# Optimization experiments

Hardware: AMD Instinct MI355X
Metric: run time of the kernel (lower is better)

The kernel has to match this reference:

```python
import jax, jax.numpy as jnp
import numpy as np

LOG2 = float(np.log(2.0))
CUTOFF = 10.0
NUM_G = 50
NUM_MOLS = 512


def ssp(x):
    # ShiftedSoftplus: softplus(x) - log(2)
    return jax.nn.softplus(x) - LOG2


def setup_inputs() -> dict:
    key = jax.random.key(0)
    ks = jax.random.split(key, 12)
    MOLS, ATOMS, K, H, F, G, L = NUM_MOLS, 64, 32, 128, 128, NUM_G, 6
    N = MOLS * ATOMS
    # structured radius graph: node i connects to (local+1..K) mod ATOMS in its molecule
    node = np.arange(N)
    mol = node // ATOMS
    loc = node % ATOMS
    dlt = np.arange(1, K + 1)
    src = ((loc[:, None] + dlt[None, :]) % ATOMS + mol[:, None] * ATOMS).reshape(-1)
    dst = np.repeat(node, K)
    edge_index = jnp.asarray(np.stack([src, dst]), dtype=jnp.int32)  # [2, E]
    z = jax.random.randint(ks[0], (N,), 0, 100, dtype=jnp.int32)
    # positions in a 5A cube -> all intra-molecule dists < cutoff=10
    pos = jax.random.uniform(ks[1], (N, 3), dtype=jnp.float32) * 5.0
    batch = jnp.asarray(mol, dtype=jnp.int32)

    def nrm(k, shape, scale):
        return jax.random.normal(k, shape, dtype=jnp.float32) * scale

    return dict(
        z=z, pos=pos, batch=batch, edge_index=edge_index,
        emb=nrm(ks[2], (100, H), 1.0),
        mlp_w1=nrm(ks[3], (L, G, F), 0.14),
        mlp_b1=jnp.zeros((L, F), jnp.float32),
        mlp_w2=nrm(ks[4], (L, F, F), 0.09),
        mlp_b2=jnp.zeros((L, F), jnp.float32),
        conv_w1=nrm(ks[5], (L, H, F), 0.09),
        conv_w2=nrm(ks[6], (L, F, H), 0.09),
        conv_b2=jnp.zeros((L, H), jnp.float32),
        lin_w=nrm(ks[7], (L, H, H), 0.09),
        lin_b=jnp.zeros((L, H), jnp.float32),
        out_w1=nrm(ks[8], (H, H // 2), 0.1),
        out_b1=jnp.zeros((H // 2,), jnp.float32),
        out_w2=nrm(ks[9], (H // 2, 1), 0.15),
        out_b2=jnp.zeros((1,), jnp.float32),
    )


def reference(z, pos, batch, edge_index, emb, mlp_w1, mlp_b1, mlp_w2, mlp_b2,
              conv_w1, conv_w2, conv_b2, lin_w, lin_b,
              out_w1, out_b1, out_w2, out_b2):
    N = pos.shape[0]
    src, dst = edge_index[0], edge_index[1]  # source j -> target i
    h = emb[z]                                                 # [N,H]
    d = jnp.linalg.norm(pos[dst] - pos[src], axis=-1)          # [E]
    # GaussianSmearing(start=0, stop=cutoff, num_gaussians)
    offset = jnp.linspace(0.0, CUTOFF, NUM_G)
    coeff = -0.5 / (offset[1] - offset[0]) ** 2
    edge_attr = jnp.exp(coeff * (d[:, None] - offset[None, :]) ** 2)  # [E,G]
    # cosine cutoff
    C = 0.5 * (jnp.cos(d * jnp.pi / CUTOFF) + 1.0)             # [E]
    L = mlp_w1.shape[0]
    for l in range(L):  # fixed small layer count
        # filter MLP on edge features, modulated by cutoff
        W = (ssp(edge_attr @ mlp_w1[l] + mlp_b1[l]) @ mlp_w2[l] + mlp_b2[l]) * C[:, None]  # [E,F]
        hx = h @ conv_w1[l]                                    # lin1 (no bias) [N,F]
        msg = hx[src] * W                                      # gather + modulate [E,F]
        agg = jax.ops.segment_sum(msg, dst, num_segments=N)    # scatter-add [N,F]
        v = agg @ conv_w2[l] + conv_b2[l]                      # lin2
        v = ssp(v) @ lin_w[l] + lin_b[l]                       # act + lin
        h = h + v                                              # residual
    h = ssp(h @ out_w1 + out_b1)
    h = h @ out_w2 + out_b2                                    # [N,1]
    out = jax.ops.segment_sum(h, batch, num_segments=NUM_MOLS) # per-molecule 'add' readout
    return out
```

## Files before the change

kernel.cpp:

```cpp
#include <hip/hip_runtime.h>
#include <math.h>

#define NN 32768
#define HH 128
#define GG 50
#define KK 32
#define LL 6
#define MM 512
#define TT 2048
#define TROWS 2049
#define ROWB 256

typedef _Float16 f16x8 __attribute__((ext_vector_type(8)));
typedef float    f32x4 __attribute__((ext_vector_type(4)));

__device__ __forceinline__ float ssp(float x) {
  return fmaxf(x, 0.f) + __logf(1.f + __expf(-fabsf(x))) - 0.69314718055994530942f;
}

__global__ __launch_bounds__(256)
void setup_all(const float* __restrict__ cw1, const float* __restrict__ cw2,
               const float* __restrict__ lw, _Float16* __restrict__ cwT,
               const float* __restrict__ mw1, const float* __restrict__ mw2,
               const float* __restrict__ mb1, const float* __restrict__ mb2,
               const float* __restrict__ ow1,
               _Float16* __restrict__ o1hT, _Float16* __restrict__ o1lT,
               char* __restrict__ Vtb) {
  int b = blockIdx.x;
  int tid = threadIdx.x;

  if (b < 72) {
    __shared__ float t[32][33];
    int wid = b >> 2, tj = b & 3;
    int l = wid / 3, m = wid % 3;
    const float* w = ((m == 0) ? cw1 : (m == 1) ? cw2 : lw) + (size_t)l * 16384;
    _Float16* o = cwT + (size_t)wid * 16384;
    int tx = tid & 31, ty = tid >> 5;
    for (int tf = 0; tf < 4; ++tf) {
      __syncthreads();
      for (int r = ty; r < 32; r += 8) t[r][tx] = w[(size_t)(tj*32 + r)*128 + tf*32 + tx];
      __syncthreads();
      for (int r = ty; r < 32; r += 8)
        o[(size_t)(tf*32 + r)*128 + tj*32 + tx] = (_Float16)t[tx][r];
    }
    return;
  }
  if (b < 76) {
    __shared__ float t[32][33];
    int tj = b - 72;
    int tx = tid & 31, ty = tid >> 5;
    for (int tf = 0; tf < 2; ++tf) {
      __syncthreads();
      for (int r = ty; r < 32; r += 8) t[r][tx] = ow1[(size_t)(tj*32 + r)*64 + tf*32 + tx];
      __syncthreads();
      for (int r = ty; r < 32; r += 8) {
        float v = t[tx][r];
        _Float16 h = (_Float16)v;
        size_t oi = (size_t)(tf*32 + r)*128 + tj*32 + tx;
        o1hT[oi] = h;
        o1lT[oi] = (_Float16)(v - (float)h);
      }
    }
    return;
  }

  __shared__ _Float16 eah[16][72], eal[16][72];
  __shared__ _Float16 t1h[16][136], t1l[16][136];

  int bb = b - 76;
  int l  = bb / 129;
  int rb = (bb % 129) * 16;
  int wave = tid >> 6, lane = tid & 63;
  int q = lane >> 4, c = lane & 15;

  const float DSTEP = 10.f / (float)TT;
  const float GSTEP = 10.f / 49.f;
  const float COEFF = -0.5f * 4.9f * 4.9f;

  for (int o = tid; o < 16*64; o += 256) {
    int r = o >> 6, g = o & 63;
    float d = (float)(rb + r) * DSTEP;
    float tt = d - (float)g * GSTEP;
    float v = (g < GG) ? __expf(COEFF * tt * tt) : 0.f;
    _Float16 h = (_Float16)v;
    eah[r][g] = h;
    eal[r][g] = (_Float16)(v - (float)h);
  }
  __syncthreads();

  #pragma unroll
  for (int tI = 0; tI < 2; ++tI) {
    int col = (wave*2 + tI)*16 + c;
    f32x4 a = {0.f, 0.f, 0.f, 0.f};
    #pragma unroll
    for (int kk = 0; kk < 2; ++kk) {
      f16x8 bh, bl;
      #pragma unroll
      for (int i = 0; i < 8; ++i) {
        int k = kk*32 + q*8 + i;
        float v = (k < GG) ? mw1[((size_t)l*GG + k)*128 + col] : 0.f;
        _Float16 h = (_Float16)v;
        bh[i] = h;
        bl[i] = (_Float16)(v - (float)h);
      }
      f16x8 ah = *(const f16x8*)&eah[c][kk*32 + q*8];
      f16x8 al = *(const f16x8*)&eal[c][kk*32 + q*8];
      a = __builtin_amdgcn_mfma_f32_16x16x32_f16(ah, bh, a, 0, 0, 0);
      a = __builtin_amdgcn_mfma_f32_16x16x32_f16(ah, bl, a, 0, 0, 0);
      a = __builtin_amdgcn_mfma_f32_16x16x32_f16(al, bh, a, 0, 0, 0);
    }
    float bv = mb1[l*128 + col];
    #pragma unroll
    for (int r = 0; r < 4; ++r) {
      float v = ssp(a[r] + bv);
      _Float16 h = (_Float16)v;
      t1h[q*4 + r][col] = h;
      t1l[q*4 + r][col] = (_Float16)(v - (float)h);
    }
  }
  __syncthreads();

  #pragma unroll
  for (int tI = 0; tI < 2; ++tI) {
    int col = (wave*2 + tI)*16 + c;
    f32x4 a = {0.f, 0.f, 0.f, 0.f};
    #pragma unroll
    for (int kk = 0; kk < 4; ++kk) {
      f16x8 bh, bl;
      #pragma unroll
      for (int i = 0; i < 8; ++i) {
        int k = kk*32 + q*8 + i;
        float v = mw2[((size_t)l*128 + k)*128 + col];
        _Float16 h = (_Float16)v;
        bh[i] = h;
        bl[i] = (_Float16)(v - (float)h);
      }
      f16x8 ah = *(const f16x8*)&t1h[c][kk*32 + q*8];
      f16x8 al = *(const f16x8*)&t1l[c][kk*32 + q*8];
      a = __builtin_amdgcn_mfma_f32_16x16x32_f16(ah, bh, a, 0, 0, 0);
      a = __builtin_amdgcn_mfma_f32_16x16x32_f16(ah, bl, a, 0, 0, 0);
      a = __builtin_amdgcn_mfma_f32_16x16x32_f16(al, bh, a, 0, 0, 0);
    }
    float bv = mb2[l*128 + col];
    #pragma unroll
    for (int r = 0; r < 4; ++r) {
      int rr = rb + q*4 + r;
      if (rr <= TT) {
        float d = (float)rr * DSTEP;
        float Cc = 0.5f * (__cosf(d * 0.31415926535897931f) + 1.f);
        ((_Float16*)(Vtb + ((size_t)l*TROWS + rr) * ROWB))[col] = (_Float16)((a[r] + bv) * Cc);
      }
    }
  }
}

__device__ __forceinline__ void wave_gemm(const _Float16 (*__restrict__ A)[136],
                                          const _Float16* __restrict__ B,
                                          int c, int q, int n0, f32x4* res) {
  f16x8 bf[4];
  #pragma unroll
  for (int kk = 0; kk < 4; ++kk)
    bf[kk] = *(const f16x8*)&B[(size_t)(n0 + c)*128 + kk*32 + q*8];
  #pragma unroll
  for (int m = 0; m < 4; ++m) {
    f32x4 a = {0.f, 0.f, 0.f, 0.f};
    #pragma unroll
    for (int kk = 0; kk < 4; ++kk) {
      f16x8 av = *(const f16x8*)&A[m*16 + c][kk*32 + q*8];
      a = __builtin_amdgcn_mfma_f32_16x16x32_f16(av, bf[kk], a, 0, 0, 0);
    }
    res[m] = a;
  }
}

__global__ __launch_bounds__(512, 4)
void mega_kernel(const int* __restrict__ z, const float* __restrict__ pos,
                 const float* __restrict__ emb,
                 const _Float16* __restrict__ cwT,
                 const float* __restrict__ cb2, const float* __restrict__ lb,
                 const char* __restrict__ Vtb,
                 const _Float16* __restrict__ o1hT, const _Float16* __restrict__ o1lT,
                 const float* __restrict__ ob1,
                 const float* __restrict__ ow2, const float* __restrict__ ob2,
                 float* __restrict__ out) {
  __shared__ _Float16     hcur[64][136];
  __shared__ _Float16     sb[64][136];
  __shared__ _Float16     hxs[64][136];
  __shared__ float        posL[64][4];
  __shared__ unsigned int edata[64*33];
  __shared__ float        red2[2][64];

  int tid = threadIdx.x;
  int wave = tid >> 6, lane = tid & 63;
  int q = lane >> 4, c = lane & 15;
  int n0 = wave * 16;
  int mol = blockIdx.x, gbase = mol * 64;

  if (tid < 192) posL[tid / 3][tid % 3] = pos[(size_t)gbase*3 + tid];
  for (int o = tid; o < 64*64; o += 512) {
    int n = o >> 6, p2 = (o & 63) * 2;
    float2 ev = *(const float2*)&emb[(size_t)z[gbase + n]*128 + p2];
    hcur[n][p2]     = (_Float16)ev.x;
    hcur[n][p2 + 1] = (_Float16)ev.y;
  }
  __syncthreads();

  for (int e = tid; e < 2048; e += 512) {
    int n = e >> 5, k = e & 31;
    int s = (n + k + 1) & 63;
    float dx = posL[n][0] - posL[s][0];
    float dy = posL[n][1] - posL[s][1];
    float dz = posL[n][2] - posL[s][2];
    float d = sqrtf(dx*dx + dy*dy + dz*dz);
    int idx = (int)(d * ((float)TT / 10.f) + 0.5f);
    edata[n*33 + k] = (unsigned int)idx << 8;
  }
  __syncthreads();

  int en = tid >> 3, ej = tid & 7;
  int f0 = ej * 8;

  for (int l = 0; l < LL; ++l) {
    {
      f32x4 res[4];
      wave_gemm(hcur, cwT + (size_t)(l*3 + 0)*16384, c, q, n0, res);
      #pragma unroll
      for (int m = 0; m < 4; ++m)
        #pragma unroll
        for (int r = 0; r < 4; ++r)
          hxs[m*16 + q*4 + r][n0 + c] = (_Float16)res[m][r];
    }
    __syncthreads();

    f16x8 accA0 = {0,0,0,0,0,0,0,0}, accA1 = accA0;
    f16x8 accB0 = accA0, accB1 = accA0;
    const char* Vl = Vtb + (size_t)l * TROWS * ROWB + f0*2;
    #pragma unroll 4
    for (int k = 0; k < KK; ++k) {
      unsigned int off = edata[en*33 + k];
      int s = (en + k + 1) & 63;
      const char* p = Vl + off;
      f16x8 va = *(const f16x8*)p;
      f16x8 vb = *(const f16x8*)(p + 128);
      f16x8 ha = *(const f16x8*)&hxs[s][f0];
      f16x8 hb = *(const f16x8*)&hxs[s][f0 + 64];
      if (k & 1) { accA1 = ha * va + accA1; accB1 = hb * vb + accB1; }
      else       { accA0 = ha * va + accA0; accB0 = hb * vb + accB0; }
    }
    *(f16x8*)&sb[en][f0]      = accA0 + accA1;
    *(f16x8*)&sb[en][f0 + 64] = accB0 + accB1;
    __syncthreads();

    {
      f32x4 vres[4];
      wave_gemm(sb, cwT + (size_t)(l*3 + 1)*16384, c, q, n0, vres);
      float b2v = cb2[l*128 + n0 + c];
      #pragma unroll
      for (int m = 0; m < 4; ++m)
        #pragma unroll
        for (int r = 0; r < 4; ++r)
          hxs[m*16 + q*4 + r][n0 + c] = (_Float16)ssp(vres[m][r] + b2v);
    }
    __syncthreads();

    {
      f32x4 res[4];
      wave_gemm(hxs, cwT + (size_t)(l*3 + 2)*16384, c, q, n0, res);
      float lbv = lb[l*128 + n0 + c];
      #pragma unroll
      for (int m = 0; m < 4; ++m)
        #pragma unroll
        for (int r = 0; r < 4; ++r) {
          int row = m*16 + q*4 + r;
          float h = (float)hcur[row][n0 + c];
          hcur[row][n0 + c] = (_Float16)(h + res[m][r] + lbv);
        }
    }
    __syncthreads();
  }

  {
    int mt = wave & 3, nh = wave >> 2;
    float pr[4] = {0.f, 0.f, 0.f, 0.f};
    #pragma unroll
    for (int tI = 0; tI < 2; ++tI) {
      int col = (nh*2 + tI)*16 + c;
      f32x4 a = {0.f, 0.f, 0.f, 0.f};
      #pragma unroll
      for (int kk = 0; kk < 4; ++kk) {
        f16x8 av = *(const f16x8*)&hcur[mt*16 + c][kk*32 + q*8];
        f16x8 bh = *(const f16x8*)&o1hT[(size_t)col*128 + kk*32 + q*8];
        f16x8 bl = *(const f16x8*)&o1lT[(size_t)col*128 + kk*32 + q*8];
        a = __builtin_amdgcn_mfma_f32_16x16x32_f16(av, bh, a, 0, 0, 0);
        a = __builtin_amdgcn_mfma_f32_16x16x32_f16(av, bl, a, 0, 0, 0);
      }
      float o2 = ow2[col], b1 = ob1[col];
      #pragma unroll
      for (int r = 0; r < 4; ++r) pr[r] += ssp(a[r] + b1) * o2;
    }
    #pragma unroll
    for (int off = 1; off < 16; off <<= 1)
      #pragma unroll
      for (int r = 0; r < 4; ++r) pr[r] += __shfl_xor(pr[r], off, 64);
    if (c == 0) {
      #pragma unroll
      for (int r = 0; r < 4; ++r) red2[nh][mt*16 + q*4 + r] = pr[r];
    }
  }
  __syncthreads();
  if (tid < 64) {
    float v = red2[0][tid] + red2[1][tid];
    #pragma unroll
    for (int off = 1; off < 64; off <<= 1) v += __shfl_xor(v, off, 64);
    if (tid == 0) out[mol] = v + 64.f * ob2[0];
  }
}

extern "C" void kernel_launch(void* const* d_in, const int* in_sizes, int n_in,
                              void* d_out, int out_size, void* d_ws, size_t ws_size,
                              hipStream_t stream) {
  const int*   z       = (const int*)d_in[0];
  const float* pos     = (const float*)d_in[1];
  const float* emb     = (const float*)d_in[4];
  const float* mlp_w1  = (const float*)d_in[5];
  const float* mlp_b1  = (const float*)d_in[6];
  const float* mlp_w2  = (const float*)d_in[7];
  const float* mlp_b2  = (const float*)d_in[8];
  const float* conv_w1 = (const float*)d_in[9];
  const float* conv_w2 = (const float*)d_in[10];
  const float* conv_b2 = (const float*)d_in[11];
  const float* lin_w   = (const float*)d_in[12];
  const float* lin_b   = (const float*)d_in[13];
  const float* out_w1  = (const float*)d_in[14];
  const float* out_b1  = (const float*)d_in[15];
  const float* out_w2  = (const float*)d_in[16];
  const float* out_b2  = (const float*)d_in[17];

  char*     Vtb  = (char*)d_ws;
  _Float16* cwT  = (_Float16*)(Vtb + (size_t)LL*TROWS*ROWB);
  _Float16* o1hT = cwT  + (size_t)18*16384;
  _Float16* o1lT = o1hT + (size_t)64*128;

  setup_all<<<76 + LL*129, 256, 0, stream>>>(conv_w1, conv_w2, lin_w, cwT,
      mlp_w1, mlp_w2, mlp_b1, mlp_b2, out_w1, o1hT, o1lT, Vtb);
  mega_kernel<<<MM, 512, 0, stream>>>(z, pos, emb, cwT, conv_b2, lin_b,
      Vtb, o1hT, o1lT, out_b1, out_w2, out_b2, (float*)d_out);
}
```

Measured before the change: 207.0 us.

## Remap message aggregation so each wave consumes only its own GEMM columns, dropping a barrier

Reassigns the edge-aggregation work so each wave handles the same feature columns it just wrote in the hxs GEMM epilogue, covering all 64 nodes with two node rows per lane. This lets the block-wide barrier between the lin1 GEMM and the gather-multiply loop be removed. The aim is to cut synchronization stalls per layer. The cost is a different LDS access pattern for hxs and edata that may cause more bank conflicts, and correctness relies on the column ownership lining up exactly with the GEMM's n0 mapping.

```diff
diff --git a/kernel.cpp b/kernel.cpp
--- a/kernel.cpp
+++ b/kernel.cpp
@@ -217,8 +217,8 @@
   }
   __syncthreads();
 
-  int en = tid >> 3, ej = tid & 7;
-  int f0 = ej * 8;
+  int n1 = lane & 31, cc = lane >> 5;
+  int fcE = n0 + cc * 8;
 
   for (int l = 0; l < LL; ++l) {
     {
@@ -230,25 +230,27 @@
         for (int r = 0; r < 4; ++r)
           hxs[m*16 + q*4 + r][n0 + c] = (_Float16)res[m][r];
     }
-    __syncthreads();
-
-    f16x8 accA0 = {0,0,0,0,0,0,0,0}, accA1 = accA0;
-    f16x8 accB0 = accA0, accB1 = accA0;
-    const char* Vl = Vtb + (size_t)l * TROWS * ROWB + f0*2;
-    #pragma unroll 4
-    for (int k = 0; k < KK; ++k) {
-      unsigned int off = edata[en*33 + k];
-      int s = (en + k + 1) & 63;
-      const char* p = Vl + off;
-      f16x8 va = *(const f16x8*)p;
-      f16x8 vb = *(const f16x8*)(p + 128);
-      f16x8 ha = *(const f16x8*)&hxs[s][f0];
-      f16x8 hb = *(const f16x8*)&hxs[s][f0 + 64];
-      if (k & 1) { accA1 = ha * va + accA1; accB1 = hb * vb + accB1; }
-      else       { accA0 = ha * va + accA0; accB0 = hb * vb + accB0; }
-    }
-    *(f16x8*)&sb[en][f0]      = accA0 + accA1;
-    *(f16x8*)&sb[en][f0 + 64] = accB0 + accB1;
+
+    {
+      f16x8 a10 = {0,0,0,0,0,0,0,0}, a11 = a10;
+      f16x8 a20 = a10, a21 = a10;
+      const char* Vl = Vtb + (size_t)l * TROWS * ROWB + fcE*2;
+      const unsigned int* e1 = &edata[n1*33];
+      const unsigned int* e2 = &edata[(n1 + 32)*33];
+      #pragma unroll 4
+      for (int k = 0; k < KK; ++k) {
+        int s1 = (n1 + k + 1) & 63;
+        int s2 = (s1 + 32) & 63;
+        f16x8 h1 = *(const f16x8*)&hxs[s1][fcE];
+        f16x8 h2 = *(const f16x8*)&hxs[s2][fcE];
+        f16x8 v1 = *(const f16x8*)(Vl + e1[k]);
+        f16x8 v2 = *(const f16x8*)(Vl + e2[k]);
+        if (k & 1) { a11 = h1 * v1 + a11; a21 = h2 * v2 + a21; }
+        else       { a10 = h1 * v1 + a10; a20 = h2 * v2 + a20; }
+      }
+      *(f16x8*)&sb[n1][fcE]      = a10 + a11;
+      *(f16x8*)&sb[n1 + 32][fcE] = a20 + a21;
+    }
     __syncthreads();
 
     {
```

Result: slower. 324.7 us (+56.9%).
